# Kernel tuning notes

Measured on AMD Instinct MI355X. Metric: run time of the kernel, lower is better.

## Reference

```python
import jax, jax.numpy as jnp
import numpy as np

B = 262144
MA = [128, 128]
MB = [128, 128]


def krone_linear(x_a, x_b, wa, wb, ba, bb):
    # slice inputs to each branch's in_features (torch slices the wider branch)
    ia, ib = wa.shape[1], wb.shape[1]
    x_a = x_a[:, :ia]
    x_b = x_b[:, :ib]
    h_a = x_a @ wa.T + ba
    h_b = x_b @ wb.T + bb
    # zero-pad the narrower output so both branches share a width (static shapes)
    oa, ob = wa.shape[0], wb.shape[0]
    if oa > ob:
        h_b = jnp.pad(h_b, ((0, 0), (0, oa - ob)))
    elif ob > oa:
        h_a = jnp.pad(h_a, ((0, 0), (0, ob - oa)))
    return h_a, h_b


def krone_softmax(x_a, x_b, fa, fb):
    x_a = x_a[:, :fa]
    x_b = x_b[:, :fb]
    # vectorized per-row Kronecker product: kron(a, b)[i*fb + j] = a[i]*b[j]
    y = (x_a[:, :, None] * x_b[:, None, :]).reshape(x_a.shape[0], fa * fb)
    return jax.nn.softmax(y, axis=1)


def setup_inputs() -> dict:
    key = jax.random.key(0)
    ks = jax.random.split(key, 13)
    s = 0.1
    inp = {
        "x": jax.random.normal(ks[0], (2, B, 2), dtype=jnp.float32),
        "w1a": jax.random.normal(ks[1], (MA[0], 2), dtype=jnp.float32) * s,
        "w1b": jax.random.normal(ks[2], (MB[0], 2), dtype=jnp.float32) * s,
        "b1a": jax.random.normal(ks[3], (MA[0],), dtype=jnp.float32) * s,
        "b1b": jax.random.normal(ks[4], (MB[0],), dtype=jnp.float32) * s,
        "w2a": jax.random.normal(ks[5], (MA[1], MA[0]), dtype=jnp.float32) * s,
        "w2b": jax.random.normal(ks[6], (MB[1], MB[0]), dtype=jnp.float32) * s,
        "b2a": jax.random.normal(ks[7], (MA[1],), dtype=jnp.float32) * s,
        "b2b": jax.random.normal(ks[8], (MB[1],), dtype=jnp.float32) * s,
        "w3a": jax.random.normal(ks[9], (1, MA[1]), dtype=jnp.float32) * s,
        "w3b": jax.random.normal(ks[10], (3, MB[1]), dtype=jnp.float32) * s,
        "b3a": jax.random.normal(ks[11], (1,), dtype=jnp.float32) * s,
        "b3b": jax.random.normal(ks[12], (3,), dtype=jnp.float32) * s,
    }
    return inp


def reference(x, w1a, w1b, b1a, b1b, w2a, w2b, b2a, b2b, w3a, w3b, b3a, b3b):
    x_a, x_b = x[0], x[1]
    h_a, h_b = krone_linear(x_a, x_b, w1a, w1b, b1a, b1b)
    h_a, h_b = jax.nn.relu(h_a), jax.nn.relu(h_b)
    h_a, h_b = krone_linear(h_a, h_b, w2a, w2b, b2a, b2b)
    h_a, h_b = jax.nn.relu(h_a), jax.nn.relu(h_b)
    h_a, h_b = krone_linear(h_a, h_b, w3a, w3b, b3a, b3b)
    return krone_softmax(h_a, h_b, 1, 3)
```

## Files before the change

kernel.cpp:

```cpp
#include <hip/hip_runtime.h>
#include <hip/hip_bf16.h>


#define BTOT 262144
#define NBLK (BTOT / 512)

typedef __attribute__((ext_vector_type(4))) float floatx4;
typedef __attribute__((ext_vector_type(8))) short bf16x8;
typedef __attribute__((ext_vector_type(4))) int  intx4;

#define OFF_W2  0
#define OFF_W1  32768
#define OFF_B2  35072
#define OFF_W3  35584
#define OFF_SA  37120
#define LDS_TOTAL 39168

static __device__ __forceinline__ int pack2bf(float lo, float hi) {
    unsigned a = __builtin_bit_cast(unsigned, lo) + 0x8000u;
    unsigned b = __builtin_bit_cast(unsigned, hi) + 0x8000u;
    return (int)__builtin_amdgcn_perm(b, a, 0x07060302u);
}

#define SEL4(a0, a1, a2, a3, i) \
    ((i) == 0 ? (a0) : (i) == 1 ? (a1) : (i) == 2 ? (a2) : (a3))

static __device__ __forceinline__ float redcol(float v) {
    v += __shfl_xor(v, 1); v += __shfl_xor(v, 2);
    v += __shfl_xor(v, 4); v += __shfl_xor(v, 8);
    return v;
}

static __device__ __forceinline__ int w1slot(int k) { return k + (k >> 3); }

static __device__ __forceinline__ void pack_path(
        unsigned char* smem, int tid,
        const float* __restrict__ w2, const float* __restrict__ w1,
        const float* __restrict__ b1, const float* __restrict__ b2) {
    const float4* w2p = (const float4*)w2;
    #pragma unroll
    for (int i = 0; i < 8; ++i) {
        int n  = (tid & 15) | (i << 4);
        int k4 = tid >> 4;
        float4 f = w2p[n * 32 + k4];
        int k = k4 * 4;
        int s = k >> 5;
        int j0 = k & 7;
        int l = ((k & 31) >> 3) * 16 + (n & 15);
        int2 pkd;
        pkd.x = pack2bf(f.x, f.y);
        pkd.y = pack2bf(f.z, f.w);
        *(int2*)(smem + OFF_W2 + (s * 8 + (n >> 4)) * 1024 + l * 16 + j0 * 2) = pkd;
    }
    if (tid < 128) {
        ((float4*)(smem + OFF_W1))[w1slot(tid)] =
            make_float4(w1[2 * tid], w1[2 * tid + 1], b1[tid], 0.f);
        ((float*)(smem + OFF_B2))[tid] = b2[tid];
    }
}

#define GEMM_CHUNK(acc, XV, W1p, W2p, B2p)                                     \
    {                                                                          \
        _Pragma("unroll")                                                      \
        for (int t = 0; t < 8; ++t) {                                          \
            float b2n = (B2p)[t * 16 + col];                                   \
            floatx4 bi = (floatx4){b2n, b2n, b2n, b2n};                        \
            _Pragma("unroll")                                                  \
            for (int mt = 0; mt < 2; ++mt) acc[t][mt] = bi;                    \
        }                                                                      \
        _Pragma("unroll")                                                      \
        for (int s = 0; s < 4; ++s) {                                          \
            intx4 af[2];                                                       \
            const int bslot = s * 36 + quad * 9;                               \
            _Pragma("unroll")                                                  \
            for (int j2 = 0; j2 < 4; ++j2) {                                   \
                float4 c0 = (W1p)[bslot + 2 * j2];                             \
                float4 c1 = (W1p)[bslot + 2 * j2 + 1];                         \
                _Pragma("unroll")                                              \
                for (int mt = 0; mt < 2; ++mt) {                               \
                    float h0 = fmaxf(fmaf((XV)[mt].x, c0.x,                    \
                                fmaf((XV)[mt].y, c0.y, c0.z)), 0.f);           \
                    float h1 = fmaxf(fmaf((XV)[mt].x, c1.x,                    \
                                fmaf((XV)[mt].y, c1.y, c1.z)), 0.f);           \
                    af[mt][j2] = pack2bf(h0, h1);                              \
                }                                                              \
            }                                                                  \
            _Pragma("unroll")                                                  \
            for (int t = 0; t < 8; ++t) {                                      \
                bf16x8 bfr = (W2p)[(s * 8 + t) * 64 + lane];                   \
                _Pragma("unroll")                                              \
                for (int mt = 0; mt < 2; ++mt)                                 \
                    acc[t][mt] = __builtin_amdgcn_mfma_f32_16x16x32_bf16(      \
                        __builtin_bit_cast(bf16x8, af[mt]), bfr,               \
                        acc[t][mt], 0, 0, 0);                                  \
            }                                                                  \
        }                                                                      \
    }

__global__ __launch_bounds__(512, 4)
void krone_fused(const float* __restrict__ x,
                 const float* __restrict__ w1a, const float* __restrict__ w1b,
                 const float* __restrict__ b1a, const float* __restrict__ b1b,
                 const float* __restrict__ w2a, const float* __restrict__ w2b,
                 const float* __restrict__ b2a, const float* __restrict__ b2b,
                 const float* __restrict__ w3a, const float* __restrict__ w3b,
                 const float* __restrict__ b3a, const float* __restrict__ b3b,
                 float* __restrict__ out) {
    __shared__ __align__(16) unsigned char smem[LDS_TOTAL];

    const int tid  = threadIdx.x;
    const int lane = tid & 63;
    const int wave = tid >> 6;
    const int quad = lane >> 4;
    const int col  = lane & 15;
    const int wbase = blockIdx.x * 512 + wave * 64;

    const bf16x8* W2 = (const bf16x8*)(smem + OFF_W2);
    const float4* W1 = (const float4*)(smem + OFF_W1);
    const float*  B2 = (const float*)(smem + OFF_B2);
    const float*  W3 = (const float*)(smem + OFF_W3);
    float*        SA = (float*)(smem + OFF_SA);
    const float2* xA = (const float2*)x;
    const float2* xB = xA + BTOT;

    const float b3a_ = b3a[0];
    const float b30 = b3b[0], b31 = b3b[1], b32 = b3b[2];

    float2 xv[4];
    #pragma unroll
    for (int c = 0; c < 2; ++c)
        #pragma unroll
        for (int mt = 0; mt < 2; ++mt)
            xv[c * 2 + mt] = xA[wbase + c * 32 + mt * 16 + col];

    pack_path(smem, tid, w2a, w1a, b1a, b2a);
    if (tid < 128) ((float*)(smem + OFF_W3))[tid] = w3a[tid];
    __syncthreads();

    #pragma unroll
    for (int c = 0; c < 2; ++c) {
        __builtin_amdgcn_sched_barrier(0);
        floatx4 acc[8][2];
        GEMM_CHUNK(acc, xv + 2 * c, W1, W2, B2);
        __builtin_amdgcn_sched_barrier(0);

        float pa[2][4] = {};
        #pragma unroll
        for (int t = 0; t < 8; ++t) {
            float w3n = W3[t * 16 + col];
            #pragma unroll
            for (int mt = 0; mt < 2; ++mt)
                #pragma unroll
                for (int r = 0; r < 4; ++r)
                    pa[mt][r] = fmaf(w3n, fmaxf(acc[t][mt][r], 0.f), pa[mt][r]);
        }
        #pragma unroll
        for (int mt = 0; mt < 2; ++mt)
            #pragma unroll
            for (int r = 0; r < 4; ++r) pa[mt][r] = redcol(pa[mt][r]);
        __builtin_amdgcn_sched_barrier(0);

        if (col < 4) {
            #pragma unroll
            for (int mt = 0; mt < 2; ++mt) {
                int sl = mt * 16 + quad * 4 + col;
                SA[wave * 64 + c * 32 + sl] =
                    SEL4(pa[mt][0], pa[mt][1], pa[mt][2], pa[mt][3], col) + b3a_;
            }
        }
        __builtin_amdgcn_sched_barrier(0);
    }

    #pragma unroll
    for (int c = 0; c < 2; ++c)
        #pragma unroll
        for (int mt = 0; mt < 2; ++mt)
            xv[c * 2 + mt] = xB[wbase + c * 32 + mt * 16 + col];

    __syncthreads();
    pack_path(smem, tid, w2b, w1b, b1b, b2b);
    if (tid < 384) ((float*)(smem + OFF_W3))[tid] = w3b[tid];
    __syncthreads();

    #pragma unroll
    for (int c = 0; c < 2; ++c) {
        __builtin_amdgcn_sched_barrier(0);
        floatx4 acc[8][2];
        GEMM_CHUNK(acc, xv + 2 * c, W1, W2, B2);
        __builtin_amdgcn_sched_barrier(0);

        #pragma unroll
        for (int mt = 0; mt < 2; ++mt) {
            float p0[4] = {}, p1[4] = {}, p2[4] = {};
            #pragma unroll
            for (int t = 0; t < 8; ++t) {
                int n = t * 16 + col;
                float w30 = W3[n], w31 = W3[128 + n], w32 = W3[256 + n];
                #pragma unroll
                for (int r = 0; r < 4; ++r) {
                    float h = fmaxf(acc[t][mt][r], 0.f);
                    p0[r] = fmaf(w30, h, p0[r]);
                    p1[r] = fmaf(w31, h, p1[r]);
                    p2[r] = fmaf(w32, h, p2[r]);
                }
            }
            #pragma unroll
            for (int r = 0; r < 4; ++r) {
                p0[r] = redcol(p0[r]);
                p1[r] = redcol(p1[r]);
                p2[r] = redcol(p2[r]);
            }
            if (col < 4) {
                int sl = mt * 16 + quad * 4 + col;
                float t0 = SEL4(p0[0], p0[1], p0[2], p0[3], col) + b30;
                float t1 = SEL4(p1[0], p1[1], p1[2], p1[3], col) + b31;
                float t2 = SEL4(p2[0], p2[1], p2[2], p2[3], col) + b32;
                float sa = SA[wave * 64 + c * 32 + sl];
                float y0 = sa * t0, y1 = sa * t1, y2 = sa * t2;
                float m = fmaxf(y0, fmaxf(y1, y2));
                float e0 = __expf(y0 - m), e1 = __expf(y1 - m), e2 = __expf(y2 - m);
                float rs = 1.f / (e0 + e1 + e2);
                long o = (long)(wbase + c * 32 + sl) * 3;
                out[o]     = e0 * rs;
                out[o + 1] = e1 * rs;
                out[o + 2] = e2 * rs;
            }
        }
        __builtin_amdgcn_sched_barrier(0);
    }
}

extern "C" void kernel_launch(void* const* d_in, const int* in_sizes, int n_in,
                              void* d_out, int out_size, void* d_ws, size_t ws_size,
                              hipStream_t stream) {
    const float* x   = (const float*)d_in[0];
    const float* w1a = (const float*)d_in[1];
    const float* w1b = (const float*)d_in[2];
    const float* b1a = (const float*)d_in[3];
    const float* b1b = (const float*)d_in[4];
    const float* w2a = (const float*)d_in[5];
    const float* w2b = (const float*)d_in[6];
    const float* b2a = (const float*)d_in[7];
    const float* b2b = (const float*)d_in[8];
    const float* w3a = (const float*)d_in[9];
    const float* w3b = (const float*)d_in[10];
    const float* b3a = (const float*)d_in[11];
    const float* b3b = (const float*)d_in[12];
    float* out = (float*)d_out;

    krone_fused<<<NBLK, 512, 0, stream>>>(x, w1a, w1b, b1a, b1b, w2a, w2b,
                                          b2a, b2b, w3a, w3b, b3a, b3b, out);
}
```

Measured before the change: 111.2 us.

## Stage both branch weights into LDS upfront and vectorize FMAs with packed float2

Both branches' W2 (bf16), W1/b1, b2 and w3 weights are packed into a larger LDS region in a single prologue. This removes the mid-kernel pair of barriers and the second weight repack between the A and B branches. The layer-1 and epilogue arithmetic is rewritten with float2/float4 elementwise FMA/max so the compiler can emit packed FP32 ops (v_pk_fma_f32), and the column reductions are batched. The cost is LDS use rising from about 39KB to about 73KB per block, which can cut the number of resident 512-thread blocks per CU and conflicts with the launch_bounds occupancy target of 4.

```diff
diff --git a/kernel.cpp b/kernel.cpp
--- a/kernel.cpp
+++ b/kernel.cpp
@@ -5,16 +5,18 @@
 #define BTOT 262144
 #define NBLK (BTOT / 512)
 
+typedef __attribute__((ext_vector_type(2))) float floatx2;
 typedef __attribute__((ext_vector_type(4))) float floatx4;
 typedef __attribute__((ext_vector_type(8))) short bf16x8;
 typedef __attribute__((ext_vector_type(4))) int  intx4;
 
 #define OFF_W2  0
-#define OFF_W1  32768
-#define OFF_B2  35072
-#define OFF_W3  35584
-#define OFF_SA  37120
-#define LDS_TOTAL 39168
+#define OFF_W1  65536
+#define OFF_B2  68608
+#define OFF_W3A 69632
+#define OFF_W3B 70144
+#define OFF_SA  71680
+#define LDS_TOTAL 73728
 
 static __device__ __forceinline__ int pack2bf(float lo, float hi) {
     unsigned a = __builtin_bit_cast(unsigned, lo) + 0x8000u;
@@ -22,67 +24,52 @@
     return (int)__builtin_amdgcn_perm(b, a, 0x07060302u);
 }
 
-#define SEL4(a0, a1, a2, a3, i) \
-    ((i) == 0 ? (a0) : (i) == 1 ? (a1) : (i) == 2 ? (a2) : (a3))
-
-static __device__ __forceinline__ float redcol(float v) {
-    v += __shfl_xor(v, 1); v += __shfl_xor(v, 2);
-    v += __shfl_xor(v, 4); v += __shfl_xor(v, 8);
+#define SEL4(v, i) \
+    ((i) == 0 ? (v).x : (i) == 1 ? (v).y : (i) == 2 ? (v).z : (v).w)
+
+static __device__ __forceinline__ floatx4 redcol4(floatx4 v) {
+    #pragma unroll
+    for (int m = 1; m <= 8; m <<= 1) {
+        floatx4 t;
+        t.x = __shfl_xor(v.x, m);
+        t.y = __shfl_xor(v.y, m);
+        t.z = __shfl_xor(v.z, m);
+        t.w = __shfl_xor(v.w, m);
+        v = v + t;
+    }
     return v;
 }
 
-static __device__ __forceinline__ int w1slot(int k) { return k + (k >> 3); }
-
-static __device__ __forceinline__ void pack_path(
-        unsigned char* smem, int tid,
-        const float* __restrict__ w2, const float* __restrict__ w1,
-        const float* __restrict__ b1, const float* __restrict__ b2) {
-    const float4* w2p = (const float4*)w2;
-    #pragma unroll
-    for (int i = 0; i < 8; ++i) {
-        int n  = (tid & 15) | (i << 4);
-        int k4 = tid >> 4;
-        float4 f = w2p[n * 32 + k4];
-        int k = k4 * 4;
-        int s = k >> 5;
-        int j0 = k & 7;
-        int l = ((k & 31) >> 3) * 16 + (n & 15);
-        int2 pkd;
-        pkd.x = pack2bf(f.x, f.y);
-        pkd.y = pack2bf(f.z, f.w);
-        *(int2*)(smem + OFF_W2 + (s * 8 + (n >> 4)) * 1024 + l * 16 + j0 * 2) = pkd;
-    }
-    if (tid < 128) {
-        ((float4*)(smem + OFF_W1))[w1slot(tid)] =
-            make_float4(w1[2 * tid], w1[2 * tid + 1], b1[tid], 0.f);
-        ((float*)(smem + OFF_B2))[tid] = b2[tid];
-    }
-}
-
-#define GEMM_CHUNK(acc, XV, W1p, W2p, B2p)                                     \
+static __device__ __forceinline__ floatx4 splat4(float s) {
+    return (floatx4){s, s, s, s};
+}
+
+#define GEMM_CHUNK(acc, XV, W1P, W2p, B2p)                                     \
     {                                                                          \
         _Pragma("unroll")                                                      \
         for (int t = 0; t < 8; ++t) {                                          \
             float b2n = (B2p)[t * 16 + col];                                   \
-            floatx4 bi = (floatx4){b2n, b2n, b2n, b2n};                        \
+            floatx4 bi = splat4(b2n);                                          \
             _Pragma("unroll")                                                  \
             for (int mt = 0; mt < 2; ++mt) acc[t][mt] = bi;                    \
         }                                                                      \
         _Pragma("unroll")                                                      \
         for (int s = 0; s < 4; ++s) {                                          \
             intx4 af[2];                                                       \
-            const int bslot = s * 36 + quad * 9;                               \
             _Pragma("unroll")                                                  \
             for (int j2 = 0; j2 < 4; ++j2) {                                   \
-                float4 c0 = (W1p)[bslot + 2 * j2];                             \
-                float4 c1 = (W1p)[bslot + 2 * j2 + 1];                         \
+                int kp = s * 16 + quad * 4 + j2;                               \
+                floatx2 w0p = (W1P)[kp * 3];                                   \
+                floatx2 w1p = (W1P)[kp * 3 + 1];                               \
+                floatx2 b1p = (W1P)[kp * 3 + 2];                               \
                 _Pragma("unroll")                                              \
                 for (int mt = 0; mt < 2; ++mt) {                               \
-                    float h0 = fmaxf(fmaf((XV)[mt].x, c0.x,                    \
-                                fmaf((XV)[mt].y, c0.y, c0.z)), 0.f);           \
-                    float h1 = fmaxf(fmaf((XV)[mt].x, c1.x,                    \
-                                fmaf((XV)[mt].y, c1.y, c1.z)), 0.f);           \
-                    af[mt][j2] = pack2bf(h0, h1);                              \
+                    floatx2 xx = (floatx2){(XV)[mt].x, (XV)[mt].x};            \
+                    floatx2 xy = (floatx2){(XV)[mt].y, (XV)[mt].y};            \
+                    floatx2 h = __builtin_elementwise_fma(xx, w0p,             \
+                                  __builtin_elementwise_fma(xy, w1p, b1p));    \
+                    h = __builtin_elementwise_max(h, (floatx2){0.f, 0.f});     \
+                    af[mt][j2] = pack2bf(h.x, h.y);                            \
                 }                                                              \
             }                                                                  \
             _Pragma("unroll")                                                  \
@@ -115,13 +102,53 @@
     const int col  = lane & 15;
     const int wbase = blockIdx.x * 512 + wave * 64;
 
-    const bf16x8* W2 = (const bf16x8*)(smem + OFF_W2);
-    const float4* W1 = (const float4*)(smem + OFF_W1);
-    const float*  B2 = (const float*)(smem + OFF_B2);
-    const float*  W3 = (const float*)(smem + OFF_W3);
-    float*        SA = (float*)(smem + OFF_SA);
-    const float2* xA = (const float2*)x;
-    const float2* xB = xA + BTOT;
+    {
+        #pragma unroll
+        for (int i = 0; i < 16; ++i) {
+            const int path = i >> 3;
+            const float4* w2p = (const float4*)(path ? w2b : w2a);
+            int n  = (tid & 15) | ((i & 7) << 4);
+            int k4 = tid >> 4;
+            float4 f = w2p[n * 32 + k4];
+            int k = k4 * 4;
+            int s = k >> 5;
+            int j0 = k & 7;
+            int l = ((k & 31) >> 3) * 16 + (n & 15);
+            int2 pkd;
+            pkd.x = pack2bf(f.x, f.y);
+            pkd.y = pack2bf(f.z, f.w);
+            *(int2*)(smem + OFF_W2 + path * 32768 +
+                     (s * 8 + (n >> 4)) * 1024 + l * 16 + j0 * 2) = pkd;
+        }
+        if (tid < 128) {
+            int p = tid >> 6, kp = tid & 63;
+            const float* w1 = p ? w1b : w1a;
+            const float* b1 = p ? b1b : b1a;
+            float4 w4 = ((const float4*)w1)[kp];
+            floatx2* dst = (floatx2*)(smem + OFF_W1) + p * 192 + kp * 3;
+            dst[0] = (floatx2){w4.x, w4.z};
+            dst[1] = (floatx2){w4.y, w4.w};
+            dst[2] = (floatx2){b1[2 * kp], b1[2 * kp + 1]};
+            ((float*)(smem + OFF_B2))[tid] = b2a[tid];
+            ((float*)(smem + OFF_W3A))[tid] = w3a[tid];
+        } else if (tid < 256) {
+            ((float*)(smem + OFF_B2))[tid] = b2b[tid - 128];
+        }
+        if (tid >= 128)
+            ((float*)(smem + OFF_W3B))[tid - 128] = w3b[tid - 128];
+    }
+
+    const bf16x8*  W2A = (const bf16x8*)(smem + OFF_W2);
+    const bf16x8*  W2B = (const bf16x8*)(smem + OFF_W2 + 32768);
+    const floatx2* W1A = (const floatx2*)(smem + OFF_W1);
+    const floatx2* W1B = W1A + 192;
+    const float*   B2A = (const float*)(smem + OFF_B2);
+    const float*   B2B = B2A + 128;
+    const float*   W3A = (const float*)(smem + OFF_W3A);
+    const float*   W3B = (const float*)(smem + OFF_W3B);
+    float*         SA  = (float*)(smem + OFF_SA);
+    const float2*  xA  = (const float2*)x;
+    const float2*  xB  = xA + BTOT;
 
     const float b3a_ = b3a[0];
     const float b30 = b3b[0], b31 = b3b[1], b32 = b3b[2];
@@ -133,39 +160,35 @@
         for (int mt = 0; mt < 2; ++mt)
             xv[c * 2 + mt] = xA[wbase + c * 32 + mt * 16 + col];
 
-    pack_path(smem, tid, w2a, w1a, b1a, b2a);
-    if (tid < 128) ((float*)(smem + OFF_W3))[tid] = w3a[tid];
     __syncthreads();
 
     #pragma unroll
     for (int c = 0; c < 2; ++c) {
         __builtin_amdgcn_sched_barrier(0);
         floatx4 acc[8][2];
-        GEMM_CHUNK(acc, xv + 2 * c, W1, W2, B2);
-        __builtin_amdgcn_sched_barrier(0);
-
-        float pa[2][4] = {};
+        GEMM_CHUNK(acc, xv + 2 * c, W1A, W2A, B2A);
+        __builtin_amdgcn_sched_barrier(0);
+
+        floatx4 pa[2] = {(floatx4){0.f,0.f,0.f,0.f}, (floatx4){0.f,0.f,0.f,0.f}};
         #pragma unroll
         for (int t = 0; t < 8; ++t) {
-            float w3n = W3[t * 16 + col];
+            floatx4 w4 = splat4(W3A[t * 16 + col]);
             #pragma unroll
-            for (int mt = 0; mt < 2; ++mt)
-                #pragma unroll
-                for (int r = 0; r < 4; ++r)
-                    pa[mt][r] = fmaf(w3n, fmaxf(acc[t][mt][r], 0.f), pa[mt][r]);
-        }
-        #pragma unroll
-        for (int mt = 0; mt < 2; ++mt)
-            #pragma unroll
-            for (int r = 0; r < 4; ++r) pa[mt][r] = redcol(pa[mt][r]);
+            for (int mt = 0; mt < 2; ++mt) {
+                floatx4 h = __builtin_elementwise_max(acc[t][mt],
+                                                      (floatx4){0.f,0.f,0.f,0.f});
+                pa[mt] = __builtin_elementwise_fma(w4, h, pa[mt]);
+            }
+        }
+        #pragma unroll
+        for (int mt = 0; mt < 2; ++mt) pa[mt] = redcol4(pa[mt]);
         __builtin_amdgcn_sched_barrier(0);
 
         if (col < 4) {
             #pragma unroll
             for (int mt = 0; mt < 2; ++mt) {
                 int sl = mt * 16 + quad * 4 + col;
-                SA[wave * 64 + c * 32 + sl] =
-                    SEL4(pa[mt][0], pa[mt][1], pa[mt][2], pa[mt][3], col) + b3a_;
+                SA[wave * 64 + c * 32 + sl] = SEL4(pa[mt], col) + b3a_;
             }
         }
         __builtin_amdgcn_sched_barrier(0);
@@ -177,44 +200,32 @@
         for (int mt = 0; mt < 2; ++mt)
             xv[c * 2 + mt] = xB[wbase + c * 32 + mt * 16 + col];
 
-    __syncthreads();
-    pack_path(smem, tid, w2b, w1b, b1b, b2b);
-    if (tid < 384) ((float*)(smem + OFF_W3))[tid] = w3b[tid];
-    __syncthreads();
-
     #pragma unroll
     for (int c = 0; c < 2; ++c) {
         __builtin_amdgcn_sched_barrier(0);
         floatx4 acc[8][2];
-        GEMM_CHUNK(acc, xv + 2 * c, W1, W2, B2);
+        GEMM_CHUNK(acc, xv + 2 * c, W1B, W2B, B2B);
         __builtin_amdgcn_sched_barrier(0);
 
         #pragma unroll
         for (int mt = 0; mt < 2; ++mt) {
-            float p0[4] = {}, p1[4] = {}, p2[4] = {};
+            floatx4 p0 = (floatx4){0.f,0.f,0.f,0.f};
+            floatx4 p1 = p0, p2 = p0;
             #pragma unroll
             for (int t = 0; t < 8; ++t) {
                 int n = t * 16 + col;
-                float w30 = W3[n], w31 = W3[128 + n], w32 = W3[256 + n];
-                #pragma unroll
-                for (int r = 0; r < 4; ++r) {
-                    float h = fmaxf(acc[t][mt][r], 0.f);
-                    p0[r] = fmaf(w30, h, p0[r]);
-                    p1[r] = fmaf(w31, h, p1[r]);
-                    p2[r] = fmaf(w32, h, p2[r]);
-                }
-            }
-            #pragma unroll
-            for (int r = 0; r < 4; ++r) {
-                p0[r] = redcol(p0[r]);
-                p1[r] = redcol(p1[r]);
-                p2[r] = redcol(p2[r]);
-            }
+                floatx4 h = __builtin_elementwise_max(acc[t][mt],
+                                                      (floatx4){0.f,0.f,0.f,0.f});
+                p0 = __builtin_elementwise_fma(splat4(W3B[n]),       h, p0);
+                p1 = __builtin_elementwise_fma(splat4(W3B[128 + n]), h, p1);
+                p2 = __builtin_elementwise_fma(splat4(W3B[256 + n]), h, p2);
+            }
+            p0 = redcol4(p0); p1 = redcol4(p1); p2 = redcol4(p2);
             if (col < 4) {
                 int sl = mt * 16 + quad * 4 + col;
-                float t0 = SEL4(p0[0], p0[1], p0[2], p0[3], col) + b30;
-                float t1 = SEL4(p1[0], p1[1], p1[2], p1[3], col) + b31;
-                float t2 = SEL4(p2[0], p2[1], p2[2], p2[3], col) + b32;
+                float t0 = SEL4(p0, col) + b30;
+                float t1 = SEL4(p1, col) + b31;
+                float t2 = SEL4(p2, col) + b32;
                 float sa = SA[wave * 64 + c * 32 + sl];
                 float y0 = sa * t0, y1 = sa * t1, y2 = sa * t2;
                 float m = fmaxf(y0, fmaxf(y1, y2));
```

Result: no change. 113.1 us (+1.6%).
